# Kernel optimization log

Measured on AMD Instinct MI355X. Metric: run time of the kernel, lower is better.

Reference implementation:

```python
import jax, jax.numpy as jnp
import numpy as np

W = 1e-4  # connectivity weight from __init__


def _box27(pred):
    """Periodic 3x3x3 neighbor sum over the last three (spatial) axes.

    Equivalent to sum of torch.roll(pred, s, (1,2,3)) over all 27 shifts
    s in {-1,0,1}^3, computed separably (3 rolls per axis instead of 27).
    pred: int8 [B, C, D, H, W]; result values in [0, 27] (fits int8).
    """
    acc = pred
    for ax in (2, 3, 4):
        acc = acc + jnp.roll(acc, 1, axis=ax) + jnp.roll(acc, -1, axis=ax)
    return acc


def setup_inputs() -> dict:
    key = jax.random.key(0)
    k1, k2 = jax.random.split(key)
    B, C, D, H, Wd = 4, 1, 192, 192, 192
    x = jax.random.normal(k1, (B, C, D, H, Wd), dtype=jnp.float32)
    y = jax.random.uniform(k2, (B, C, D, H, Wd), dtype=jnp.float32)
    is_gt = jnp.ones((B,), dtype=jnp.float32)
    return {"x": x, "y": y, "is_gt": is_gt}


def reference(x, y, is_gt):
    # pred = (x > 0) as int8, matching torch .type(torch.int8)
    pred = (x > 0).astype(jnp.int8)
    acc = _box27(pred)  # [B,C,D,H,W], values 0..27
    # connectivity term: fraction of voxels where 27-neighbor sum equals pred
    conn = jnp.mean((acc == pred).astype(jnp.float32), axis=(1, 2, 3, 4))  # [B]
    # BCEWithLogitsLoss (mean reduction, numerically stable form)
    bce = jnp.mean(
        jnp.maximum(x, 0.0) - x * y + jnp.log1p(jnp.exp(-jnp.abs(x))),
        axis=(1, 2, 3, 4),
    )  # [B]
    loss = jnp.sum(is_gt * bce + W * conn)
    return loss.reshape(1)
```

## Files before the change

kernel.cpp:

```cpp
#include <hip/hip_runtime.h>
#include <cstdint>

#define NB    4
#define DD    192
#define HH    192
#define WW    192
#define WPR   6
#define NPB   (DD*HH*WW)
#define NWORDS (NB*DD*HH*WPR)
#define W_CONN 1e-4f

__global__ __launch_bounds__(256) void k_bce_pack(
    const float* __restrict__ x, const float* __restrict__ y,
    uint32_t* __restrict__ bits, float* __restrict__ bce_sum)
{
    const int w = blockIdx.x * 256 + threadIdx.x;
    const long base = (long)w * 32;
    const float4* __restrict__ x4 = reinterpret_cast<const float4*>(x + base);
    const float4* __restrict__ y4 = reinterpret_cast<const float4*>(y + base);

    float s = 0.0f;
    uint32_t m = 0;
#pragma unroll
    for (int j = 0; j < 8; ++j) {
        const float4 xv = x4[j];
        const float4 yv = y4[j];
        {   float xi = xv.x, yi = yv.x;
            s += fmaxf(xi, 0.0f) - xi * yi + log1pf(__expf(-fabsf(xi)));
            m |= (xi > 0.0f ? 1u : 0u) << (4 * j + 0); }
        {   float xi = xv.y, yi = yv.y;
            s += fmaxf(xi, 0.0f) - xi * yi + log1pf(__expf(-fabsf(xi)));
            m |= (xi > 0.0f ? 1u : 0u) << (4 * j + 1); }
        {   float xi = xv.z, yi = yv.z;
            s += fmaxf(xi, 0.0f) - xi * yi + log1pf(__expf(-fabsf(xi)));
            m |= (xi > 0.0f ? 1u : 0u) << (4 * j + 2); }
        {   float xi = xv.w, yi = yv.w;
            s += fmaxf(xi, 0.0f) - xi * yi + log1pf(__expf(-fabsf(xi)));
            m |= (xi > 0.0f ? 1u : 0u) << (4 * j + 3); }
    }
    bits[w] = m;

    __shared__ float red[256];
    red[threadIdx.x] = s;
    __syncthreads();
#pragma unroll
    for (int off = 128; off > 0; off >>= 1) {
        if (threadIdx.x < off) red[threadIdx.x] += red[threadIdx.x + off];
        __syncthreads();
    }
    if (threadIdx.x == 0) {
        const int b = (int)(base / (long)NPB);
        atomicAdd(&bce_sum[b], red[0]);
    }
}

__global__ __launch_bounds__(256) void k_conn(
    const uint32_t* __restrict__ bits, unsigned int* __restrict__ conn_cnt)
{
    const int w = blockIdx.x * 256 + threadIdx.x;
    const int wi  = w % WPR;
    const int t1  = w / WPR;
    const int yy  = t1 % HH;
    const int t2  = t1 / HH;
    const int zz  = t2 % DD;
    const int b   = t2 / DD;

    const int wiL = (wi == 0)       ? (WPR - 1) : (wi - 1);
    const int wiR = (wi == WPR - 1) ? 0         : (wi + 1);

    const uint32_t* __restrict__ bb = bits + (long)b * (DD * HH * WPR);

    uint32_t n26 = 0;
#pragma unroll
    for (int dz = -1; dz <= 1; ++dz) {
#pragma unroll
        for (int dy = -1; dy <= 1; ++dy) {
            int z2 = zz + dz; if (z2 < 0) z2 += DD; if (z2 >= DD) z2 -= DD;
            int y2 = yy + dy; if (y2 < 0) y2 += HH; if (y2 >= HH) y2 -= HH;
            const uint32_t* row = bb + ((long)z2 * HH + y2) * WPR;
            const uint32_t c = row[wi];
            const uint32_t l = row[wiL];
            const uint32_t r = row[wiR];
            uint32_t o = ((c << 1) | (l >> 31)) | ((c >> 1) | (r << 31));
            if (!(dz == 0 && dy == 0)) o |= c;
            n26 |= o;
        }
    }
    int cnt = 32 - __popc(n26);

    __shared__ int red[256];
    red[threadIdx.x] = cnt;
    __syncthreads();
#pragma unroll
    for (int off = 128; off > 0; off >>= 1) {
        if (threadIdx.x < off) red[threadIdx.x] += red[threadIdx.x + off];
        __syncthreads();
    }
    if (threadIdx.x == 0) {
        atomicAdd(&conn_cnt[b], (unsigned int)red[0]);
    }
}

__global__ void k_final(const float* __restrict__ is_gt,
                        const float* __restrict__ bce_sum,
                        const unsigned int* __restrict__ conn_cnt,
                        float* __restrict__ out)
{
    if (threadIdx.x == 0 && blockIdx.x == 0) {
        const float inv = 1.0f / (float)NPB;
        float loss = 0.0f;
#pragma unroll
        for (int b = 0; b < NB; ++b) {
            loss += is_gt[b] * (bce_sum[b] * inv)
                  + W_CONN  * ((float)conn_cnt[b] * inv);
        }
        out[0] = loss;
    }
}

extern "C" void kernel_launch(void* const* d_in, const int* in_sizes, int n_in,
                              void* d_out, int out_size, void* d_ws, size_t ws_size,
                              hipStream_t stream) {
    const float* x     = (const float*)d_in[0];
    const float* y     = (const float*)d_in[1];
    const float* is_gt = (const float*)d_in[2];
    float* out = (float*)d_out;

    char* ws = (char*)d_ws;
    float*        bce_sum  = (float*)ws;
    unsigned int* conn_cnt = (unsigned int*)(ws + 64);
    uint32_t*     bits     = (uint32_t*)(ws + 256);

    hipMemsetAsync(ws, 0, 256, stream);

    const int blocks = NWORDS / 256;
    k_bce_pack<<<blocks, 256, 0, stream>>>(x, y, bits, bce_sum);
    k_conn   <<<blocks, 256, 0, stream>>>(bits, conn_cnt);
    k_final  <<<1, 64, 0, stream>>>(is_gt, bce_sum, conn_cnt, out);
}
```

Before: 313.3 us.

## Coalesce BCE pass with one float4 per thread and wave-ballot bit packing

Each thread now loads a single float4 of x and y, so consecutive lanes read consecutive addresses, replacing the old per-thread 128-byte strided chunk. The sign bits are gathered with four wave ballots and interleaved back into 32-bit words with a bit-spread helper, and lanes 0-7 write the packed words. The softplus term also switches to hardware exp2/log intrinsics, which trades some accuracy for fewer instructions. The grid for the first kernel grows eightfold, which increases block-reduction and atomic traffic.

```diff
diff --git a/kernel.cpp b/kernel.cpp
--- a/kernel.cpp
+++ b/kernel.cpp
@@ -8,37 +8,60 @@
 #define WPR   6
 #define NPB   (DD*HH*WW)
 #define NWORDS (NB*DD*HH*WPR)
+#define NELEM (NB*NPB)
 #define W_CONN 1e-4f
 
+__device__ __forceinline__ uint32_t spread4(uint32_t x) {
+    x = (x | (x << 12)) & 0x000F000Fu;
+    x = (x | (x << 6))  & 0x03030303u;
+    x = (x | (x << 3))  & 0x11111111u;
+    return x;
+}
+
+__device__ __forceinline__ float softplus_neg_abs(float a) {
+    const float LOG2E = 1.44269504088896340736f;
+    const float LN2   = 0.69314718055994530942f;
+    float t = __builtin_amdgcn_exp2f(-fabsf(a) * LOG2E);
+    return __builtin_amdgcn_logf(1.0f + t) * LN2;
+}
+
 __global__ __launch_bounds__(256) void k_bce_pack(
-    const float* __restrict__ x, const float* __restrict__ y,
+    const float4* __restrict__ x4, const float4* __restrict__ y4,
     uint32_t* __restrict__ bits, float* __restrict__ bce_sum)
 {
-    const int w = blockIdx.x * 256 + threadIdx.x;
-    const long base = (long)w * 32;
-    const float4* __restrict__ x4 = reinterpret_cast<const float4*>(x + base);
-    const float4* __restrict__ y4 = reinterpret_cast<const float4*>(y + base);
+    const int tid = blockIdx.x * 256 + threadIdx.x;
+    const float4 xv = x4[tid];
+    const float4 yv = y4[tid];
 
     float s = 0.0f;
-    uint32_t m = 0;
-#pragma unroll
-    for (int j = 0; j < 8; ++j) {
-        const float4 xv = x4[j];
-        const float4 yv = y4[j];
-        {   float xi = xv.x, yi = yv.x;
-            s += fmaxf(xi, 0.0f) - xi * yi + log1pf(__expf(-fabsf(xi)));
-            m |= (xi > 0.0f ? 1u : 0u) << (4 * j + 0); }
-        {   float xi = xv.y, yi = yv.y;
-            s += fmaxf(xi, 0.0f) - xi * yi + log1pf(__expf(-fabsf(xi)));
-            m |= (xi > 0.0f ? 1u : 0u) << (4 * j + 1); }
-        {   float xi = xv.z, yi = yv.z;
-            s += fmaxf(xi, 0.0f) - xi * yi + log1pf(__expf(-fabsf(xi)));
-            m |= (xi > 0.0f ? 1u : 0u) << (4 * j + 2); }
-        {   float xi = xv.w, yi = yv.w;
-            s += fmaxf(xi, 0.0f) - xi * yi + log1pf(__expf(-fabsf(xi)));
-            m |= (xi > 0.0f ? 1u : 0u) << (4 * j + 3); }
+    uint32_t nib = 0;
+    {   float xi = xv.x, yi = yv.x;
+        s += fmaxf(xi, 0.0f) - xi * yi + softplus_neg_abs(xi);
+        nib |= (xi > 0.0f) ? 1u : 0u; }
+    {   float xi = xv.y, yi = yv.y;
+        s += fmaxf(xi, 0.0f) - xi * yi + softplus_neg_abs(xi);
+        nib |= (xi > 0.0f) ? 2u : 0u; }
+    {   float xi = xv.z, yi = yv.z;
+        s += fmaxf(xi, 0.0f) - xi * yi + softplus_neg_abs(xi);
+        nib |= (xi > 0.0f) ? 4u : 0u; }
+    {   float xi = xv.w, yi = yv.w;
+        s += fmaxf(xi, 0.0f) - xi * yi + softplus_neg_abs(xi);
+        nib |= (xi > 0.0f) ? 8u : 0u; }
+
+    const uint64_t b0 = __ballot(nib & 1u);
+    const uint64_t b1 = __ballot(nib & 2u);
+    const uint64_t b2 = __ballot(nib & 4u);
+    const uint64_t b3 = __ballot(nib & 8u);
+
+    const int lane = threadIdx.x & 63;
+    const int k = lane & 7;
+    uint32_t wrd = spread4((uint32_t)(b0 >> (8 * k)) & 0xFFu)
+                 | (spread4((uint32_t)(b1 >> (8 * k)) & 0xFFu) << 1)
+                 | (spread4((uint32_t)(b2 >> (8 * k)) & 0xFFu) << 2)
+                 | (spread4((uint32_t)(b3 >> (8 * k)) & 0xFFu) << 3);
+    if (lane < 8) {
+        bits[(tid >> 6) * 8 + k] = wrd;
     }
-    bits[w] = m;
 
     __shared__ float red[256];
     red[threadIdx.x] = s;
@@ -49,7 +72,7 @@
         __syncthreads();
     }
     if (threadIdx.x == 0) {
-        const int b = (int)(base / (long)NPB);
+        const int b = (int)(((long)tid * 4) / (long)NPB);
         atomicAdd(&bce_sum[b], red[0]);
     }
 }
@@ -133,8 +156,10 @@
 
     hipMemsetAsync(ws, 0, 256, stream);
 
-    const int blocks = NWORDS / 256;
-    k_bce_pack<<<blocks, 256, 0, stream>>>(x, y, bits, bce_sum);
-    k_conn   <<<blocks, 256, 0, stream>>>(bits, conn_cnt);
-    k_final  <<<1, 64, 0, stream>>>(is_gt, bce_sum, conn_cnt, out);
+    const int blocks1 = (NELEM / 4) / 256;
+    k_bce_pack<<<blocks1, 256, 0, stream>>>(
+        (const float4*)x, (const float4*)y, bits, bce_sum);
+    const int blocks2 = NWORDS / 256;
+    k_conn  <<<blocks2, 256, 0, stream>>>(bits, conn_cnt);
+    k_final <<<1, 64, 0, stream>>>(is_gt, bce_sum, conn_cnt, out);
 }
```

Measured after the change: 561.3 us. +79.1%, slower.
